# Performance work log

Measured on AMD Instinct MI355X. Metric: run time of the kernel, lower is better.

The kernel has to match this reference:

```python
import jax, jax.numpy as jnp
import numpy as np

B, S, D, F, E, K = 2, 1024, 2048, 1024, 8, 2


def setup_inputs() -> dict:
    key = jax.random.key(0)
    ks = jax.random.split(key, 5)
    scale_x = 0.02
    return {
        "x": jax.random.normal(ks[0], (B, S, D), dtype=jnp.float32),
        "w_router": jax.random.normal(ks[1], (E, D), dtype=jnp.float32) * scale_x,
        "w_gate": jax.random.normal(ks[2], (E, F, D), dtype=jnp.float32) * scale_x,
        "w_up": jax.random.normal(ks[3], (E, F, D), dtype=jnp.float32) * scale_x,
        "w_down": jax.random.normal(ks[4], (E, D, F), dtype=jnp.float32) * scale_x,
        "top_k": K,
    }


def reference(x, w_router, w_gate, w_up, w_down, top_k):
    # Router: logits [B,S,E] -> top-k indices + softmax over top-k logits (fp32)
    logits = jnp.einsum("bsd,ed->bse", x, w_router)
    top_logits, top_idx = jax.lax.top_k(logits, top_k)          # [B,S,K]
    gates = jax.nn.softmax(top_logits.astype(jnp.float32), axis=-1)
    # SwitchGLU: per-expert gated MLP. Compute all experts densely, then gather
    # the selected expert output per token (reference-faithful math).
    h = jax.nn.silu(jnp.einsum("bsd,efd->besf", x, w_gate)) * jnp.einsum(
        "bsd,efd->besf", x, w_up
    )                                                            # [B,E,S,F]
    out_all = jnp.einsum("besf,edf->bsed", h, w_down)            # [B,S,E,D]
    y = jnp.take_along_axis(out_all, top_idx[..., None], axis=2)  # [B,S,K,D]
    return (y * gates[..., None].astype(y.dtype)).sum(axis=-2)   # [B,S,D]
```

## Files before the change

### kernel.cpp

```cpp
#include <hip/hip_runtime.h>
#include <hip/hip_bf16.h>

#define T_TOK 2048
#define DIM   2048
#define FFN   1024
#define NE    8

typedef __attribute__((ext_vector_type(8))) short bf16x8;
typedef __attribute__((ext_vector_type(8))) unsigned short u16x8;
typedef __attribute__((ext_vector_type(4))) float f32x4;

__device__ __forceinline__ unsigned short f2bf(float f) {
  __hip_bfloat16 h = __float2bfloat16(f);
  return __builtin_bit_cast(unsigned short, h);
}

__device__ __forceinline__ void gload_lds16(const unsigned short* g, unsigned short* l) {
  __builtin_amdgcn_global_load_lds(
      (const __attribute__((address_space(1))) void*)g,
      (__attribute__((address_space(3))) void*)l, 16, 0, 0);
}

__device__ __forceinline__ u16x8 cvt8(float4 a, float4 b) {
  u16x8 o;
  o[0] = f2bf(a.x); o[1] = f2bf(a.y); o[2] = f2bf(a.z); o[3] = f2bf(a.w);
  o[4] = f2bf(b.x); o[5] = f2bf(b.y); o[6] = f2bf(b.z); o[7] = f2bf(b.w);
  return o;
}

__global__ __launch_bounds__(256) void cvt4(const float* __restrict__ src,
                                            unsigned short* __restrict__ dst) {
  const int tid = blockIdx.x * 256 + threadIdx.x;
  const int nthreads = gridDim.x * 256;
  const float4* s = reinterpret_cast<const float4*>(src);
  u16x8* d = reinterpret_cast<u16x8*>(dst);
#pragma unroll
  for (int g = 0; g < 4; ++g) {
    long grp = (long)g * nthreads + tid;
    float4 a = s[grp * 2];
    float4 b = s[grp * 2 + 1];
    d[grp] = cvt8(a, b);
  }
}

__global__ __launch_bounds__(256) void router_topk(
    const float* __restrict__ x, const float* __restrict__ wr,
    int* __restrict__ top_i, float* __restrict__ top_g) {
  int t = blockIdx.x * 4 + (threadIdx.x >> 6);
  int lane = threadIdx.x & 63;
  const float4* xr = reinterpret_cast<const float4*>(x) + (size_t)t * (DIM / 4);
  const float4* wrv = reinterpret_cast<const float4*>(wr);
  float acc[NE];
#pragma unroll
  for (int e = 0; e < NE; ++e) acc[e] = 0.f;
#pragma unroll
  for (int it = 0; it < DIM / 4 / 64; ++it) {
    int d4 = it * 64 + lane;
    float4 xv = xr[d4];
#pragma unroll
    for (int e = 0; e < NE; ++e) {
      float4 wv = wrv[e * (DIM / 4) + d4];
      acc[e] += xv.x * wv.x + xv.y * wv.y + xv.z * wv.z + xv.w * wv.w;
    }
  }
#pragma unroll
  for (int off = 32; off > 0; off >>= 1) {
#pragma unroll
    for (int e = 0; e < NE; ++e) acc[e] += __shfl_xor(acc[e], off, 64);
  }
  if (lane == 0) {
    int i0 = 0; float m0 = acc[0];
#pragma unroll
    for (int e = 1; e < NE; ++e) if (acc[e] > m0) { m0 = acc[e]; i0 = e; }
    int i1 = -1; float m1 = -3.4e38f;
#pragma unroll
    for (int e = 0; e < NE; ++e) if (e != i0 && acc[e] > m1) { m1 = acc[e]; i1 = e; }
    float tv = expf(m1 - m0);
    float den = 1.f + tv;
    top_i[t * 2 + 0] = i0; top_i[t * 2 + 1] = i1;
    top_g[t * 2 + 0] = 1.f / den; top_g[t * 2 + 1] = tv / den;
  }
}

__global__ void count_offsets(const int* __restrict__ top_i,
                              int* __restrict__ offs, int* __restrict__ cursor) {
  __shared__ int cnt[NE];
  if (threadIdx.x < NE) cnt[threadIdx.x] = 0;
  __syncthreads();
  for (int i = threadIdx.x; i < T_TOK * 2; i += blockDim.x) atomicAdd(&cnt[top_i[i]], 1);
  __syncthreads();
  if (threadIdx.x == 0) {
    int s = 0;
    for (int e = 0; e < NE; ++e) { offs[e] = s; cursor[e] = s; s += cnt[e]; }
    offs[NE] = s;
  }
}

__global__ void scatter_tokens(const int* __restrict__ top_i, const float* __restrict__ top_g,
                               int* __restrict__ cursor, int* __restrict__ tok_list,
                               float* __restrict__ gate_lst, int* __restrict__ slot_lst) {
  int t = blockIdx.x * blockDim.x + threadIdx.x;
  if (t >= T_TOK) return;
#pragma unroll
  for (int s = 0; s < 2; ++s) {
    int e = top_i[t * 2 + s];
    int p = atomicAdd(&cursor[e], 1);
    tok_list[p] = t;
    gate_lst[p] = top_g[t * 2 + s];
    slot_lst[p] = s;
  }
}

__global__ __launch_bounds__(256, 4) void gateup_gemm(
    const unsigned short* __restrict__ xb, const unsigned short* __restrict__ wgb,
    const unsigned short* __restrict__ wub, const int* __restrict__ tok_list,
    const int* __restrict__ offs, unsigned short* __restrict__ hbuf,
    const float* __restrict__ wd_f32, unsigned short* __restrict__ wdb) {
  if (blockIdx.x >= FFN / 64) {
    int cb = (blockIdx.x - FFN / 64) + 4 * (blockIdx.y + 32 * blockIdx.z);
    int t = cb * 256 + threadIdx.x;
    const float4* s = reinterpret_cast<const float4*>(wd_f32);
    u16x8* d = reinterpret_cast<u16x8*>(wdb);
#pragma unroll
    for (int g = 0; g < 8; ++g) {
      long grp = (long)g * 262144 + t;
      float4 a = s[grp * 2];
      float4 b = s[grp * 2 + 1];
      d[grp] = cvt8(a, b);
    }
    return;
  }
  const int e = blockIdx.z;
  const int row0 = offs[e];
  const int n_e = offs[e + 1] - row0;
  const int mt = blockIdx.y;
  if (mt * 64 >= n_e) return;
  const int nt = blockIdx.x;

  __shared__ unsigned short As[64 * 64];
  __shared__ unsigned short Bg[64 * 64];
  __shared__ unsigned short Bu[64 * 64];

  const int tid = threadIdx.x;
  const int wid = tid >> 6;
  const int lane = tid & 63;

  const int gchunk = (((lane & 7) ^ ((lane >> 3) & 7)) << 3);

  const unsigned short* gA[2];
  int lAoff[2];
#pragma unroll
  for (int p = 0; p < 2; ++p) {
    int rt = wid * 16 + p * 8 + (lane >> 3);
    int ar = mt * 64 + rt; if (ar >= n_e) ar = n_e - 1;
    gA[p] = xb + (size_t)tok_list[row0 + ar] * DIM + gchunk;
    lAoff[p] = (wid * 16 + p * 8) * 64;
  }
  const size_t wbase = (size_t)e * FFN * DIM + (size_t)(nt * 64) * DIM;
  const unsigned short* gG[2];
  const unsigned short* gU[2];
  int lBoff[2];
#pragma unroll
  for (int p = 0; p < 2; ++p) {
    int rt = wid * 16 + p * 8 + (lane >> 3);
    gG[p] = wgb + wbase + (size_t)rt * DIM + gchunk;
    gU[p] = wub + wbase + (size_t)rt * DIM + gchunk;
    lBoff[p] = (wid * 16 + p * 8) * 64;
  }

  f32x4 accg[2][2];
  f32x4 accu[2][2];
#pragma unroll
  for (int i = 0; i < 2; ++i)
#pragma unroll
    for (int j = 0; j < 2; ++j) {
      accg[i][j] = (f32x4){0.f, 0.f, 0.f, 0.f};
      accu[i][j] = (f32x4){0.f, 0.f, 0.f, 0.f};
    }

  const int warow = (wid >> 1) * 32;
  const int wacol = (wid & 1) * 32;
  const int frow = lane & 15;
  const int eo0 = ((((lane >> 4)) ^ (lane & 7)) << 3);
  const int eo1 = (((4 + (lane >> 4)) ^ (lane & 7)) << 3);

  for (int k0 = 0; k0 < DIM; k0 += 64) {
#pragma unroll
    for (int p = 0; p < 2; ++p) {
      gload_lds16(gA[p] + k0, &As[lAoff[p]]);
      gload_lds16(gG[p] + k0, &Bg[lBoff[p]]);
      gload_lds16(gU[p] + k0, &Bu[lBoff[p]]);
    }
    __syncthreads();
#pragma unroll
    for (int kk = 0; kk < 2; ++kk) {
      const int eo = kk ? eo1 : eo0;
      bf16x8 af[2], bg[2], bu[2];
#pragma unroll
      for (int i = 0; i < 2; ++i)
        af[i] = *reinterpret_cast<const bf16x8*>(&As[(warow + i * 16 + frow) * 64 + eo]);
#pragma unroll
      for (int j = 0; j < 2; ++j) {
        bg[j] = *reinterpret_cast<const bf16x8*>(&Bg[(wacol + j * 16 + frow) * 64 + eo]);
        bu[j] = *reinterpret_cast<const bf16x8*>(&Bu[(wacol + j * 16 + frow) * 64 + eo]);
      }
#pragma unroll
      for (int i = 0; i < 2; ++i)
#pragma unroll
        for (int j = 0; j < 2; ++j) {
          accg[i][j] = __builtin_amdgcn_mfma_f32_16x16x32_bf16(af[i], bg[j], accg[i][j], 0, 0, 0);
          accu[i][j] = __builtin_amdgcn_mfma_f32_16x16x32_bf16(af[i], bu[j], accu[i][j], 0, 0, 0);
        }
    }
    __syncthreads();
  }

#pragma unroll
  for (int i = 0; i < 2; ++i) {
#pragma unroll
    for (int jj = 0; jj < 4; ++jj) {
      int r = mt * 64 + warow + i * 16 + (lane >> 4) * 4 + jj;
      if (r < n_e) {
#pragma unroll
        for (int j = 0; j < 2; ++j) {
          float g = accg[i][j][jj];
          float u = accu[i][j][jj];
          float h = (g / (1.f + __expf(-g))) * u;
          int f = nt * 64 + wacol + j * 16 + (lane & 15);
          hbuf[(size_t)(row0 + r) * FFN + f] = f2bf(h);
        }
      }
    }
  }
}

__global__ __launch_bounds__(256, 4) void down_gemm(
    const unsigned short* __restrict__ hbuf, const unsigned short* __restrict__ wdb,
    const int* __restrict__ tok_list, const float* __restrict__ gate_lst,
    const int* __restrict__ slot_lst, const int* __restrict__ offs,
    float* __restrict__ yslots) {
  const int e = blockIdx.z;
  const int row0 = offs[e];
  const int n_e = offs[e + 1] - row0;
  const int mt = blockIdx.y;
  if (mt * 64 >= n_e) return;
  const int nt = blockIdx.x;

  __shared__ unsigned short As[64 * 64];
  __shared__ unsigned short Bs[128 * 64];

  const int tid = threadIdx.x;
  const int wid = tid >> 6;
  const int lane = tid & 63;

  const int gchunk = (((lane & 7) ^ ((lane >> 3) & 7)) << 3);

  const unsigned short* gA[2];
  int lAoff[2];
#pragma unroll
  for (int p = 0; p < 2; ++p) {
    int rt = wid * 16 + p * 8 + (lane >> 3);
    int ar = mt * 64 + rt; if (ar >= n_e) ar = n_e - 1;
    gA[p] = hbuf + (size_t)(row0 + ar) * FFN + gchunk;
    lAoff[p] = (wid * 16 + p * 8) * 64;
  }
  const unsigned short* gB[4];
  int lBoff[4];
#pragma unroll
  for (int p = 0; p < 4; ++p) {
    int rt = wid * 32 + p * 8 + (lane >> 3);
    gB[p] = wdb + ((size_t)e * DIM + nt * 128 + rt) * FFN + gchunk;
    lBoff[p] = (wid * 32 + p * 8) * 64;
  }

  f32x4 acc[2][4];
#pragma unroll
  for (int i = 0; i < 2; ++i)
#pragma unroll
    for (int j = 0; j < 4; ++j) acc[i][j] = (f32x4){0.f, 0.f, 0.f, 0.f};

  const int warow = (wid >> 1) * 32;
  const int wacol = (wid & 1) * 64;
  const int frow = lane & 15;
  const int eo0 = ((((lane >> 4)) ^ (lane & 7)) << 3);
  const int eo1 = (((4 + (lane >> 4)) ^ (lane & 7)) << 3);

  for (int k0 = 0; k0 < FFN; k0 += 64) {
#pragma unroll
    for (int p = 0; p < 2; ++p) gload_lds16(gA[p] + k0, &As[lAoff[p]]);
#pragma unroll
    for (int p = 0; p < 4; ++p) gload_lds16(gB[p] + k0, &Bs[lBoff[p]]);
    __syncthreads();
#pragma unroll
    for (int kk = 0; kk < 2; ++kk) {
      const int eo = kk ? eo1 : eo0;
      bf16x8 af[2], bf[4];
#pragma unroll
      for (int i = 0; i < 2; ++i)
        af[i] = *reinterpret_cast<const bf16x8*>(&As[(warow + i * 16 + frow) * 64 + eo]);
#pragma unroll
      for (int j = 0; j < 4; ++j)
        bf[j] = *reinterpret_cast<const bf16x8*>(&Bs[(wacol + j * 16 + frow) * 64 + eo]);
#pragma unroll
      for (int i = 0; i < 2; ++i)
#pragma unroll
        for (int j = 0; j < 4; ++j)
          acc[i][j] = __builtin_amdgcn_mfma_f32_16x16x32_bf16(af[i], bf[j], acc[i][j], 0, 0, 0);
    }
    __syncthreads();
  }

#pragma unroll
  for (int i = 0; i < 2; ++i) {
#pragma unroll
    for (int jj = 0; jj < 4; ++jj) {
      int r = mt * 64 + warow + i * 16 + (lane >> 4) * 4 + jj;
      if (r < n_e) {
        int tk = tok_list[row0 + r];
        float gt = gate_lst[row0 + r];
        int sl = slot_lst[row0 + r];
        float* yrow = yslots + ((size_t)sl * T_TOK + tk) * DIM;
#pragma unroll
        for (int j = 0; j < 4; ++j) {
          int d = nt * 128 + wacol + j * 16 + (lane & 15);
          yrow[d] = gt * acc[i][j][jj];
        }
      }
    }
  }
}

__global__ void combine(const float* __restrict__ y, float* __restrict__ out) {
  int i = blockIdx.x * blockDim.x + threadIdx.x;
  int stride = gridDim.x * blockDim.x;
  const float4* y0 = reinterpret_cast<const float4*>(y);
  const float4* y1 = reinterpret_cast<const float4*>(y + (size_t)T_TOK * DIM);
  float4* o = reinterpret_cast<float4*>(out);
  for (; i < T_TOK * DIM / 4; i += stride) {
    float4 a = y0[i], b = y1[i];
    float4 r;
    r.x = a.x + b.x; r.y = a.y + b.y; r.z = a.z + b.z; r.w = a.w + b.w;
    o[i] = r;
  }
}

extern "C" void kernel_launch(void* const* d_in, const int* in_sizes, int n_in,
                              void* d_out, int out_size, void* d_ws, size_t ws_size,
                              hipStream_t stream) {
  const float* x = (const float*)d_in[0];
  const float* wr = (const float*)d_in[1];
  const float* wg = (const float*)d_in[2];
  const float* wu = (const float*)d_in[3];
  const float* wd = (const float*)d_in[4];
  float* out = (float*)d_out;

  char* ws = (char*)d_ws;
  size_t off = 0;
  auto alloc = [&](size_t bytes) {
    char* p = ws + off;
    off += (bytes + 255) & ~(size_t)255;
    return p;
  };
  unsigned short* xb   = (unsigned short*)alloc((size_t)T_TOK * DIM * 2);
  unsigned short* wgb  = (unsigned short*)alloc((size_t)NE * FFN * DIM * 2);
  unsigned short* wub  = (unsigned short*)alloc((size_t)NE * FFN * DIM * 2);
  unsigned short* wdb  = (unsigned short*)alloc((size_t)NE * DIM * FFN * 2);
  unsigned short* hbuf = (unsigned short*)alloc((size_t)T_TOK * 2 * FFN * 2);
  float* yslots        = (float*)alloc((size_t)2 * T_TOK * DIM * 4);
  int* top_i     = (int*)alloc(T_TOK * 2 * 4);
  float* top_g   = (float*)alloc(T_TOK * 2 * 4);
  int* tok_list  = (int*)alloc(T_TOK * 2 * 4);
  float* gate_lst = (float*)alloc(T_TOK * 2 * 4);
  int* slot_lst  = (int*)alloc(T_TOK * 2 * 4);
  int* offs      = (int*)alloc(64);
  int* cursor    = (int*)alloc(64);
  if (off > ws_size) return;

  cvt4<<<512, 256, 0, stream>>>(x, xb);
  cvt4<<<2048, 256, 0, stream>>>(wg, wgb);
  cvt4<<<2048, 256, 0, stream>>>(wu, wub);
  router_topk<<<T_TOK / 4, 256, 0, stream>>>(x, wr, top_i, top_g);
  count_offsets<<<1, 256, 0, stream>>>(top_i, offs, cursor);
  scatter_tokens<<<(T_TOK + 255) / 256, 256, 0, stream>>>(top_i, top_g, cursor, tok_list,
                                                          gate_lst, slot_lst);
  gateup_gemm<<<dim3(FFN / 64 + 4, 32, NE), 256, 0, stream>>>(xb, wgb, wub, tok_list, offs,
                                                              hbuf, wd, wdb);
  down_gemm<<<dim3(DIM / 128, 32, NE), 256, 0, stream>>>(hbuf, wdb, tok_list, gate_lst,
                                                         slot_lst, offs, yslots);
  combine<<<2048, 256, 0, stream>>>(yslots, out);
}
```

Measured before the change: 221.6 us.

## Load fp32 expert weights directly into LDS and convert to bf16 in-kernel

Drops the separate weight-conversion passes (gate/up cvt kernels and the fused down-weight conversion blocks) and has both GEMMs stream fp32 weights straight into LDS with a new XOR swizzle. Each tile is converted to bf16 at fragment-load time. This avoids writing and rereading bf16 weight copies, at the cost of doubling the weight bytes each tile reloads and doubling LDS footprint, which can cut occupancy. Since each weight tile is reread by many M-tiles per expert, the reread traffic rises.

After: 214.2 us. 1.03x faster.

```diff
diff --git a/kernel.cpp b/kernel.cpp
--- a/kernel.cpp
+++ b/kernel.cpp
@@ -16,6 +16,11 @@
 }
 
 __device__ __forceinline__ void gload_lds16(const unsigned short* g, unsigned short* l) {
+  __builtin_amdgcn_global_load_lds(
+      (const __attribute__((address_space(1))) void*)g,
+      (__attribute__((address_space(3))) void*)l, 16, 0, 0);
+}
+__device__ __forceinline__ void gload_lds16f(const float* g, float* l) {
   __builtin_amdgcn_global_load_lds(
       (const __attribute__((address_space(1))) void*)g,
       (__attribute__((address_space(3))) void*)l, 16, 0, 0);
@@ -28,15 +33,23 @@
   return o;
 }
 
-__global__ __launch_bounds__(256) void cvt4(const float* __restrict__ src,
-                                            unsigned short* __restrict__ dst) {
+__device__ __forceinline__ bf16x8 pack8(float4 a, float4 b) {
+  bf16x8 o;
+  o[0] = (short)f2bf(a.x); o[1] = (short)f2bf(a.y);
+  o[2] = (short)f2bf(a.z); o[3] = (short)f2bf(a.w);
+  o[4] = (short)f2bf(b.x); o[5] = (short)f2bf(b.y);
+  o[6] = (short)f2bf(b.z); o[7] = (short)f2bf(b.w);
+  return o;
+}
+
+__global__ __launch_bounds__(256) void cvt_x(const float* __restrict__ src,
+                                             unsigned short* __restrict__ dst) {
   const int tid = blockIdx.x * 256 + threadIdx.x;
-  const int nthreads = gridDim.x * 256;
   const float4* s = reinterpret_cast<const float4*>(src);
   u16x8* d = reinterpret_cast<u16x8*>(dst);
 #pragma unroll
   for (int g = 0; g < 4; ++g) {
-    long grp = (long)g * nthreads + tid;
+    long grp = (long)g * (512 * 256) + tid;
     float4 a = s[grp * 2];
     float4 b = s[grp * 2 + 1];
     d[grp] = cvt8(a, b);
@@ -112,24 +125,9 @@
 }
 
 __global__ __launch_bounds__(256, 4) void gateup_gemm(
-    const unsigned short* __restrict__ xb, const unsigned short* __restrict__ wgb,
-    const unsigned short* __restrict__ wub, const int* __restrict__ tok_list,
-    const int* __restrict__ offs, unsigned short* __restrict__ hbuf,
-    const float* __restrict__ wd_f32, unsigned short* __restrict__ wdb) {
-  if (blockIdx.x >= FFN / 64) {
-    int cb = (blockIdx.x - FFN / 64) + 4 * (blockIdx.y + 32 * blockIdx.z);
-    int t = cb * 256 + threadIdx.x;
-    const float4* s = reinterpret_cast<const float4*>(wd_f32);
-    u16x8* d = reinterpret_cast<u16x8*>(wdb);
-#pragma unroll
-    for (int g = 0; g < 8; ++g) {
-      long grp = (long)g * 262144 + t;
-      float4 a = s[grp * 2];
-      float4 b = s[grp * 2 + 1];
-      d[grp] = cvt8(a, b);
-    }
-    return;
-  }
+    const unsigned short* __restrict__ xb, const float* __restrict__ wg,
+    const float* __restrict__ wu, const int* __restrict__ tok_list,
+    const int* __restrict__ offs, unsigned short* __restrict__ hbuf) {
   const int e = blockIdx.z;
   const int row0 = offs[e];
   const int n_e = offs[e + 1] - row0;
@@ -138,15 +136,14 @@
   const int nt = blockIdx.x;
 
   __shared__ unsigned short As[64 * 64];
-  __shared__ unsigned short Bg[64 * 64];
-  __shared__ unsigned short Bu[64 * 64];
+  __shared__ float Bg[64 * 64];
+  __shared__ float Bu[64 * 64];
 
   const int tid = threadIdx.x;
   const int wid = tid >> 6;
   const int lane = tid & 63;
 
   const int gchunk = (((lane & 7) ^ ((lane >> 3) & 7)) << 3);
-
   const unsigned short* gA[2];
   int lAoff[2];
 #pragma unroll
@@ -156,16 +153,17 @@
     gA[p] = xb + (size_t)tok_list[row0 + ar] * DIM + gchunk;
     lAoff[p] = (wid * 16 + p * 8) * 64;
   }
-  const size_t wbase = (size_t)e * FFN * DIM + (size_t)(nt * 64) * DIM;
-  const unsigned short* gG[2];
-  const unsigned short* gU[2];
-  int lBoff[2];
-#pragma unroll
-  for (int p = 0; p < 2; ++p) {
-    int rt = wid * 16 + p * 8 + (lane >> 3);
-    gG[p] = wgb + wbase + (size_t)rt * DIM + gchunk;
-    gU[p] = wub + wbase + (size_t)rt * DIM + gchunk;
-    lBoff[p] = (wid * 16 + p * 8) * 64;
+  const int rloc = (wid << 2) | (lane >> 4);
+  const int sc = ((lane & 15) ^ rloc) << 2;
+  const float* gG[4];
+  const float* gU[4];
+  int lBoff[4];
+#pragma unroll
+  for (int p = 0; p < 4; ++p) {
+    size_t rr = (size_t)e * FFN + nt * 64 + p * 16 + rloc;
+    gG[p] = wg + rr * DIM + sc;
+    gU[p] = wu + rr * DIM + sc;
+    lBoff[p] = (p * 16 + (wid << 2)) * 64;
   }
 
   f32x4 accg[2][2];
@@ -181,28 +179,42 @@
   const int warow = (wid >> 1) * 32;
   const int wacol = (wid & 1) * 32;
   const int frow = lane & 15;
-  const int eo0 = ((((lane >> 4)) ^ (lane & 7)) << 3);
-  const int eo1 = (((4 + (lane >> 4)) ^ (lane & 7)) << 3);
+  const int q = lane >> 4;
+  const int eoA0 = ((q ^ (lane & 7)) << 3);
+  const int eoA1 = (((4 + q) ^ (lane & 7)) << 3);
+  int boff0[2], boff1[2];
+#pragma unroll
+  for (int kk = 0; kk < 2; ++kk) {
+    int c0 = kk * 8 + q * 2;
+    boff0[kk] = ((c0 ^ frow) << 2);
+    boff1[kk] = (((c0 + 1) ^ frow) << 2);
+  }
 
   for (int k0 = 0; k0 < DIM; k0 += 64) {
 #pragma unroll
-    for (int p = 0; p < 2; ++p) {
-      gload_lds16(gA[p] + k0, &As[lAoff[p]]);
-      gload_lds16(gG[p] + k0, &Bg[lBoff[p]]);
-      gload_lds16(gU[p] + k0, &Bu[lBoff[p]]);
+    for (int p = 0; p < 2; ++p) gload_lds16(gA[p] + k0, &As[lAoff[p]]);
+#pragma unroll
+    for (int p = 0; p < 4; ++p) {
+      gload_lds16f(gG[p] + k0, &Bg[lBoff[p]]);
+      gload_lds16f(gU[p] + k0, &Bu[lBoff[p]]);
     }
     __syncthreads();
 #pragma unroll
     for (int kk = 0; kk < 2; ++kk) {
-      const int eo = kk ? eo1 : eo0;
       bf16x8 af[2], bg[2], bu[2];
 #pragma unroll
       for (int i = 0; i < 2; ++i)
-        af[i] = *reinterpret_cast<const bf16x8*>(&As[(warow + i * 16 + frow) * 64 + eo]);
+        af[i] = *reinterpret_cast<const bf16x8*>(
+            &As[(warow + i * 16 + frow) * 64 + (kk ? eoA1 : eoA0)]);
 #pragma unroll
       for (int j = 0; j < 2; ++j) {
-        bg[j] = *reinterpret_cast<const bf16x8*>(&Bg[(wacol + j * 16 + frow) * 64 + eo]);
-        bu[j] = *reinterpret_cast<const bf16x8*>(&Bu[(wacol + j * 16 + frow) * 64 + eo]);
+        int R = (wacol + j * 16 + frow) * 64;
+        float4 g0 = *reinterpret_cast<const float4*>(&Bg[R + boff0[kk]]);
+        float4 g1 = *reinterpret_cast<const float4*>(&Bg[R + boff1[kk]]);
+        bg[j] = pack8(g0, g1);
+        float4 u0 = *reinterpret_cast<const float4*>(&Bu[R + boff0[kk]]);
+        float4 u1 = *reinterpret_cast<const float4*>(&Bu[R + boff1[kk]]);
+        bu[j] = pack8(u0, u1);
       }
 #pragma unroll
       for (int i = 0; i < 2; ++i)
@@ -235,7 +247,7 @@
 }
 
 __global__ __launch_bounds__(256, 4) void down_gemm(
-    const unsigned short* __restrict__ hbuf, const unsigned short* __restrict__ wdb,
+    const unsigned short* __restrict__ hbuf, const float* __restrict__ wd,
     const int* __restrict__ tok_list, const float* __restrict__ gate_lst,
     const int* __restrict__ slot_lst, const int* __restrict__ offs,
     float* __restrict__ yslots) {
@@ -247,14 +259,13 @@
   const int nt = blockIdx.x;
 
   __shared__ unsigned short As[64 * 64];
-  __shared__ unsigned short Bs[128 * 64];
+  __shared__ float Bs[128 * 64];
 
   const int tid = threadIdx.x;
   const int wid = tid >> 6;
   const int lane = tid & 63;
 
   const int gchunk = (((lane & 7) ^ ((lane >> 3) & 7)) << 3);
-
   const unsigned short* gA[2];
   int lAoff[2];
 #pragma unroll
@@ -264,13 +275,15 @@
     gA[p] = hbuf + (size_t)(row0 + ar) * FFN + gchunk;
     lAoff[p] = (wid * 16 + p * 8) * 64;
   }
-  const unsigned short* gB[4];
-  int lBoff[4];
-#pragma unroll
-  for (int p = 0; p < 4; ++p) {
-    int rt = wid * 32 + p * 8 + (lane >> 3);
-    gB[p] = wdb + ((size_t)e * DIM + nt * 128 + rt) * FFN + gchunk;
-    lBoff[p] = (wid * 32 + p * 8) * 64;
+  const int rloc = (wid << 2) | (lane >> 4);
+  const int sc = ((lane & 15) ^ rloc) << 2;
+  const float* gB[8];
+  int lBoff[8];
+#pragma unroll
+  for (int p = 0; p < 8; ++p) {
+    size_t rr = (size_t)e * DIM + nt * 128 + p * 16 + rloc;
+    gB[p] = wd + rr * FFN + sc;
+    lBoff[p] = (p * 16 + (wid << 2)) * 64;
   }
 
   f32x4 acc[2][4];
@@ -282,25 +295,37 @@
   const int warow = (wid >> 1) * 32;
   const int wacol = (wid & 1) * 64;
   const int frow = lane & 15;
-  const int eo0 = ((((lane >> 4)) ^ (lane & 7)) << 3);
-  const int eo1 = (((4 + (lane >> 4)) ^ (lane & 7)) << 3);
+  const int q = lane >> 4;
+  const int eoA0 = ((q ^ (lane & 7)) << 3);
+  const int eoA1 = (((4 + q) ^ (lane & 7)) << 3);
+  int boff0[2], boff1[2];
+#pragma unroll
+  for (int kk = 0; kk < 2; ++kk) {
+    int c0 = kk * 8 + q * 2;
+    boff0[kk] = ((c0 ^ frow) << 2);
+    boff1[kk] = (((c0 + 1) ^ frow) << 2);
+  }
 
   for (int k0 = 0; k0 < FFN; k0 += 64) {
 #pragma unroll
     for (int p = 0; p < 2; ++p) gload_lds16(gA[p] + k0, &As[lAoff[p]]);
 #pragma unroll
-    for (int p = 0; p < 4; ++p) gload_lds16(gB[p] + k0, &Bs[lBoff[p]]);
+    for (int p = 0; p < 8; ++p) gload_lds16f(gB[p] + k0, &Bs[lBoff[p]]);
     __syncthreads();
 #pragma unroll
     for (int kk = 0; kk < 2; ++kk) {
-      const int eo = kk ? eo1 : eo0;
       bf16x8 af[2], bf[4];
 #pragma unroll
       for (int i = 0; i < 2; ++i)
-        af[i] = *reinterpret_cast<const bf16x8*>(&As[(warow + i * 16 + frow) * 64 + eo]);
-#pragma unroll
-      for (int j = 0; j < 4; ++j)
-        bf[j] = *reinterpret_cast<const bf16x8*>(&Bs[(wacol + j * 16 + frow) * 64 + eo]);
+        af[i] = *reinterpret_cast<const bf16x8*>(
+            &As[(warow + i * 16 + frow) * 64 + (kk ? eoA1 : eoA0)]);
+#pragma unroll
+      for (int j = 0; j < 4; ++j) {
+        int R = (wacol + j * 16 + frow) * 64;
+        float4 b0 = *reinterpret_cast<const float4*>(&Bs[R + boff0[kk]]);
+        float4 b1 = *reinterpret_cast<const float4*>(&Bs[R + boff1[kk]]);
+        bf[j] = pack8(b0, b1);
+      }
 #pragma unroll
       for (int i = 0; i < 2; ++i)
 #pragma unroll
@@ -362,9 +387,6 @@
     return p;
   };
   unsigned short* xb   = (unsigned short*)alloc((size_t)T_TOK * DIM * 2);
-  unsigned short* wgb  = (unsigned short*)alloc((size_t)NE * FFN * DIM * 2);
-  unsigned short* wub  = (unsigned short*)alloc((size_t)NE * FFN * DIM * 2);
-  unsigned short* wdb  = (unsigned short*)alloc((size_t)NE * DIM * FFN * 2);
   unsigned short* hbuf = (unsigned short*)alloc((size_t)T_TOK * 2 * FFN * 2);
   float* yslots        = (float*)alloc((size_t)2 * T_TOK * DIM * 4);
   int* top_i     = (int*)alloc(T_TOK * 2 * 4);
@@ -376,16 +398,13 @@
   int* cursor    = (int*)alloc(64);
   if (off > ws_size) return;
 
-  cvt4<<<512, 256, 0, stream>>>(x, xb);
-  cvt4<<<2048, 256, 0, stream>>>(wg, wgb);
-  cvt4<<<2048, 256, 0, stream>>>(wu, wub);
+  cvt_x<<<512, 256, 0, stream>>>(x, xb);
   router_topk<<<T_TOK / 4, 256, 0, stream>>>(x, wr, top_i, top_g);
   count_offsets<<<1, 256, 0, stream>>>(top_i, offs, cursor);
   scatter_tokens<<<(T_TOK + 255) / 256, 256, 0, stream>>>(top_i, top_g, cursor, tok_list,
                                                           gate_lst, slot_lst);
-  gateup_gemm<<<dim3(FFN / 64 + 4, 32, NE), 256, 0, stream>>>(xb, wgb, wub, tok_list, offs,
-                                                              hbuf, wd, wdb);
-  down_gemm<<<dim3(DIM / 128, 32, NE), 256, 0, stream>>>(hbuf, wdb, tok_list, gate_lst,
+  gateup_gemm<<<dim3(FFN / 64, 32, NE), 256, 0, stream>>>(xb, wg, wu, tok_list, offs, hbuf);
+  down_gemm<<<dim3(DIM / 128, 32, NE), 256, 0, stream>>>(hbuf, wd, tok_list, gate_lst,
                                                          slot_lst, offs, yslots);
   combine<<<2048, 256, 0, stream>>>(yslots, out);
 }
```
